# Kernel optimization log

Measured on AMD Instinct MI355X. Metric: run time of the kernel, lower is better.

## Reference

```python
import jax, jax.numpy as jnp
import numpy as np

N = 10000      # num_nodes
E = 640000     # num_edges
D = 256        # in_channels
POOL_SIZES = [(N, 48), (48, 12), (12, 4), (4, 1)]


def gcn_conv(x, src, dst, ew, W, b, n):
    """PyG-style GCNConv with edge weights: add self-loops, symmetric norm, scatter-add."""
    loop = jnp.arange(n)
    s = jnp.concatenate([src, loop])
    d = jnp.concatenate([dst, loop])
    w = jnp.concatenate([ew, jnp.ones((n,), x.dtype)])
    deg = jax.ops.segment_sum(w, d, num_segments=n)
    dinv = jnp.where(deg > 0, deg ** -0.5, 0.0)
    norm = dinv[s] * w * dinv[d]                      # [E+N]
    h = x @ W                                         # [n, out]
    out = jax.ops.segment_sum(norm[:, None] * h[s], d, num_segments=n)
    return out + b


def diffpool(x, P):
    """Learned-assignment DiffPool: S=softmax(P); x'=S^T x; reg = mean row entropy of S."""
    S = jax.nn.softmax(P, axis=-1)                    # [n_in, n_out]
    xp = S.T @ x                                      # [n_out, feat]
    reg = jnp.mean(-jnp.sum(S * jnp.log(S + 1e-12), axis=-1))
    return xp, reg


def setup_inputs() -> dict:
    key = jax.random.key(0)
    ks = jax.random.split(key, 12)
    inp = {
        "x": jax.random.normal(ks[0], (N, D), jnp.float32),
        "edge_index": jax.random.randint(ks[1], (2, E), 0, N, jnp.int64),
        "edge_attr": jax.random.uniform(ks[2], (E, 1), jnp.float32),
        "adj": jax.random.uniform(ks[3], (N, N), jnp.float32),
        # GCNConv params (out channels hard-coded to 1 in the module)
        "W1": jax.random.normal(ks[4], (D, 1), jnp.float32) / np.sqrt(D),
        "b1": jnp.zeros((1,), jnp.float32),
        "W2": jax.random.normal(ks[5], (1, 1), jnp.float32),
        "b2": jnp.zeros((1,), jnp.float32),
    }
    for i, (ni, no) in enumerate(POOL_SIZES):
        inp[f"P{i+1}"] = jax.random.normal(ks[6 + i], (ni, no), jnp.float32) * 0.1
    return inp


def reference(x, edge_index, edge_attr, adj, W1, b1, W2, b2, P1, P2, P3, P4):
    src, dst = edge_index[0], edge_index[1]
    ew = edge_attr[:, 0]
    h1 = gcn_conv(x, src, dst, ew, W1, b1, N)                       # [N,1]
    h = jnp.concatenate([h1, gcn_conv(h1[:, -1:], src, dst, ew, W2, b2, N)], axis=-1)
    h = jnp.concatenate([h, gcn_conv(h[:, -1:], src, dst, ew, W2, b2, N)], axis=-1)  # [N,3]
    reg = jnp.float32(0.0)
    for P in (P1, P2, P3, P4):
        h, r = diffpool(h, P)
        reg = reg + r
    return (h, reg)                                                  # h: [1,3]
```

## Files before the change

### kernel.cpp

```cpp
#include <hip/hip_runtime.h>
#include <math.h>

#define NN 10000
#define EE 640000
#define DD 256
#define NBK 128
#define NPB 79
#define NWRT 256
#define EPW (EE / NWRT)
#define SLOT 48
#define CELLS (NBK * SLOT)
#define SPAN (NWRT * SLOT)
#define NDEG 64
#define EPD (EE / NDEG)
#define NTHR 512

#define OFF_DINV 0
#define OFF_XW   (NN)
#define OFF_C1   (2*NN)
#define OFF_C2   (3*NN)
#define OFF_XP   (4*NN)
#define OFF_S1   (4*NN + 160)
#define OFF_DEGP (OFF_S1 + 2*NBK*SPAN)
#define OFF_PA   (OFF_DEGP + NDEG*NN)
#define OFF_PB   (OFF_PA + NBK*NN)

__global__ __launch_bounds__(NTHR) void k1_sort_deg_xw(
    const int* __restrict__ src, const int* __restrict__ dst,
    const float* __restrict__ ew, const float* __restrict__ x,
    const float* __restrict__ W1, float* __restrict__ ws)
{
    __shared__ unsigned smem[12416];
    int tid = threadIdx.x, bid = blockIdx.x;
    int lane = tid & 63, wv = tid >> 6;
    if (bid < NWRT) {
        uint2* cells = (uint2*)smem;
        int*   curs  = (int*)(smem + 2 * CELLS);
        if (bid == 0 && tid < 160) ws[OFF_XP + tid] = 0.f;
        for (int i = tid; i < CELLS; i += NTHR) cells[i] = make_uint2(0u, 0u);
        if (tid < NBK) curs[tid] = 0;
        __syncthreads();
        int base = bid * EPW;
        for (int k = tid; k < EPW; k += NTHR) {
            int s = src[base + k], d = dst[base + k];
            float w = ew[base + k];
            int j = s / NPB, loc = s - j * NPB;
            int r = atomicAdd(&curs[j], 1);
            if (r < SLOT)
                cells[j * SLOT + r] =
                    make_uint2((unsigned)d | ((unsigned)loc << 14), __float_as_uint(w));
        }
        __syncthreads();
        uint2* S1 = (uint2*)(ws + OFF_S1);
        for (int i = tid; i < CELLS; i += NTHR) {
            int j = i / SLOT, r = i - j * SLOT;
            S1[((size_t)j * NWRT + bid) * SLOT + r] = cells[i];
        }
        if (bid < 250) {
            float4 wreg = reinterpret_cast<const float4*>(W1)[lane];
            #pragma unroll
            for (int rr = 0; rr < 5; ++rr) {
                int row = bid * 40 + wv * 5 + rr;
                float4 a = reinterpret_cast<const float4*>(x + (size_t)row * DD)[lane];
                float v = a.x*wreg.x + a.y*wreg.y + a.z*wreg.z + a.w*wreg.w;
                #pragma unroll
                for (int off = 32; off; off >>= 1) v += __shfl_xor(v, off);
                if (lane == 0) ws[OFF_XW + row] = v;
            }
        }
    } else {
        float* acc = (float*)smem;
        for (int i = tid; i < NN; i += NTHR) acc[i] = 0.f;
        __syncthreads();
        int base = (bid - NWRT) * EPD;
        for (int k = tid; k < EPD; k += NTHR)
            atomicAdd(&acc[dst[base + k]], ew[base + k]);
        __syncthreads();
        float* dp = ws + OFF_DEGP + (size_t)(bid - NWRT) * NN;
        for (int i = tid; i < NN; i += NTHR) dp[i] = acc[i];
    }
}

#define REDUCE_SLICES(PIN, NS)                                            \
    for (int n = lane; n < NPB; n += 64) {                                \
        float s = 0.f;                                                    \
        if (nbase + n < NN) {                                             \
            _Pragma("unroll")                                             \
            for (int q = 0; q < (NS); ++q)                                \
                s += (PIN)[(size_t)(wv * (NS) + q) * NN + nbase + n];     \
        }                                                                 \
        red[wv][n] = s;                                                   \
    }                                                                     \
    __syncthreads();

#define SCATTER_SPAN(POUT)                                                \
    {                                                                     \
        const uint2* span = (const uint2*)(ws + OFF_S1) + (size_t)bid * SPAN; \
        for (int k = tid; k < SPAN; k += NTHR) {                          \
            uint2 pk = span[k];                                           \
            float w = __uint_as_float(pk.y);                              \
            if (w != 0.f)                                                 \
                atomicAdd(&acc[pk.x & 0x3FFF], w * du[pk.x >> 14]);       \
        }                                                                 \
        __syncthreads();                                                  \
        float* pp = (POUT) + (size_t)bid * NN;                            \
        for (int i = tid; i < NN; i += NTHR) pp[i] = acc[i];              \
    }

__global__ __launch_bounds__(NTHR) void k2_dinv_scat1(float* __restrict__ ws)
{
    __shared__ float acc[NN];
    __shared__ float red[8][NPB];
    __shared__ float du[NPB];
    int tid = threadIdx.x, bid = blockIdx.x;
    int lane = tid & 63, wv = tid >> 6;
    int nbase = bid * NPB;
    int ncnt = min(NPB, NN - nbase);
    const float* pin = ws + OFF_DEGP;
    REDUCE_SLICES(pin, 8)
    if (tid < ncnt) {
        float tot = 1.f;
        #pragma unroll
        for (int q = 0; q < 8; ++q) tot += red[q][tid];
        float di = (tot > 0.f) ? 1.0f / sqrtf(tot) : 0.f;
        ws[OFF_DINV + nbase + tid] = di;
        du[tid] = di * ws[OFF_XW + nbase + tid];
    }
    for (int i = tid; i < NN; i += NTHR) acc[i] = 0.f;
    __syncthreads();
    SCATTER_SPAN(ws + OFF_PB)
}

__global__ __launch_bounds__(NTHR) void k_conv(
    const float* __restrict__ hin, const float* __restrict__ multp,
    const float* __restrict__ biasp, float* __restrict__ cout,
    const float* __restrict__ pin, float* __restrict__ pout,
    float* __restrict__ ws)
{
    __shared__ float acc[NN];
    __shared__ float red[8][NPB];
    __shared__ float du[NPB];
    int tid = threadIdx.x, bid = blockIdx.x;
    int lane = tid & 63, wv = tid >> 6;
    int nbase = bid * NPB;
    int ncnt = min(NPB, NN - nbase);
    REDUCE_SLICES(pin, 16)
    if (tid < ncnt) {
        float tot = 0.f;
        #pragma unroll
        for (int q = 0; q < 8; ++q) tot += red[q][tid];
        float di = ws[OFF_DINV + nbase + tid];
        float M = multp ? *multp : 1.0f;
        float cv = M * di * (tot + di * hin[nbase + tid]) + *biasp;
        cout[nbase + tid] = cv;
        du[tid] = di * cv;
    }
    for (int i = tid; i < NN; i += NTHR) acc[i] = 0.f;
    __syncthreads();
    SCATTER_SPAN(pout)
}

__global__ __launch_bounds__(NTHR) void k5_final(
    const float* __restrict__ multp, const float* __restrict__ biasp,
    const float* __restrict__ pin,
    const float* __restrict__ P1, const float* __restrict__ P2,
    const float* __restrict__ P3, float* __restrict__ ws, float* __restrict__ out)
{
    __shared__ float red[8][NPB];
    __shared__ float sc3[NPB];
    __shared__ float part[8][48][3];
    __shared__ float entW[8];
    __shared__ int sh_last;
    int tid = threadIdx.x, bid = blockIdx.x;
    int lane = tid & 63, wv = tid >> 6;
    int nbase = bid * NPB;
    int ncnt = min(NPB, NN - nbase);
    const float* c1 = ws + OFF_C1;
    const float* c2 = ws + OFF_C2;
    REDUCE_SLICES(pin, 16)
    if (tid < ncnt) {
        float tot = 0.f;
        #pragma unroll
        for (int q = 0; q < 8; ++q) tot += red[q][tid];
        float di = ws[OFF_DINV + nbase + tid];
        sc3[tid] = (*multp) * di * (tot + di * c2[nbase + tid]) + *biasp;
    }
    __syncthreads();
    float a0 = 0.f, a1 = 0.f, a2 = 0.f, ent = 0.f;
    for (int r = 0; r < 10; ++r) {
        int l = wv * 10 + r;
        if (l < ncnt) {
            int row = nbase + l;
            float pv = (lane < 48) ? P1[(size_t)row * 48 + lane] : -1e30f;
            float mx = pv;
            #pragma unroll
            for (int off = 32; off; off >>= 1) mx = fmaxf(mx, __shfl_xor(mx, off));
            float e = (lane < 48) ? expf(pv - mx) : 0.f;
            float sum = e;
            #pragma unroll
            for (int off = 32; off; off >>= 1) sum += __shfl_xor(sum, off);
            float p = e / sum;
            if (lane < 48) {
                ent -= p * logf(p + 1e-12f);
                a0 += p * c1[row];
                a1 += p * c2[row];
                a2 += p * sc3[l];
            }
        }
    }
    #pragma unroll
    for (int off = 32; off; off >>= 1) ent += __shfl_xor(ent, off);
    if (lane == 0) entW[wv] = ent;
    if (lane < 48) { part[wv][lane][0] = a0; part[wv][lane][1] = a1; part[wv][lane][2] = a2; }
    __syncthreads();
    float* xp1 = ws + OFF_XP;
    if (tid < 144) {
        int j = tid / 3, col = tid % 3;
        float sp = 0.f;
        #pragma unroll
        for (int w = 0; w < 8; ++w) sp += part[w][j][col];
        atomicAdd(&xp1[j * 3 + col], sp);
    }
    if (tid == 0) {
        float sp = 0.f;
        #pragma unroll
        for (int w = 0; w < 8; ++w) sp += entW[w];
        atomicAdd(&xp1[144], sp);
    }
    if (tid == 0) {
        __threadfence();
        int old = atomicAdd((int*)ws + OFF_XP + 152, 1);
        sh_last = (old == (int)gridDim.x - 1) ? 1 : 0;
    }
    __syncthreads();
    if (sh_last) {
        __shared__ float shXp[145];
        __shared__ float S2[48][12], xp2[12][3];
        __shared__ float S3[12][4], xp3[4][3];
        __shared__ float ent2, ent3;
        if (tid < 145) shXp[tid] = atomicAdd(&xp1[tid], 0.0f);
        if (tid == 0) { ent2 = 0.f; ent3 = 0.f; }
        __syncthreads();
        if (tid < 48) {
            float v[12], mx = -1e30f;
            #pragma unroll
            for (int j = 0; j < 12; j++) { v[j] = P2[tid * 12 + j]; mx = fmaxf(mx, v[j]); }
            float sm = 0.f;
            #pragma unroll
            for (int j = 0; j < 12; j++) { v[j] = expf(v[j] - mx); sm += v[j]; }
            float e = 0.f;
            #pragma unroll
            for (int j = 0; j < 12; j++) {
                float p = v[j] / sm; S2[tid][j] = p; e -= p * logf(p + 1e-12f);
            }
            atomicAdd(&ent2, e);
        }
        __syncthreads();
        if (tid < 36) {
            int j = tid / 3, col = tid % 3;
            float sm = 0.f;
            for (int i = 0; i < 48; i++) sm += S2[i][j] * shXp[i * 3 + col];
            xp2[j][col] = sm;
        }
        __syncthreads();
        if (tid < 12) {
            float v[4], mx = -1e30f;
            #pragma unroll
            for (int j = 0; j < 4; j++) { v[j] = P3[tid * 4 + j]; mx = fmaxf(mx, v[j]); }
            float sm = 0.f;
            #pragma unroll
            for (int j = 0; j < 4; j++) { v[j] = expf(v[j] - mx); sm += v[j]; }
            float e = 0.f;
            #pragma unroll
            for (int j = 0; j < 4; j++) {
                float p = v[j] / sm; S3[tid][j] = p; e -= p * logf(p + 1e-12f);
            }
            atomicAdd(&ent3, e);
        }
        __syncthreads();
        if (tid < 12) {
            int j = tid / 3, col = tid % 3;
            float sm = 0.f;
            for (int i = 0; i < 12; i++) sm += S3[i][j] * xp2[i][col];
            xp3[j][col] = sm;
        }
        __syncthreads();
        if (tid == 0) {
            float o0 = 0.f, o1 = 0.f, o2 = 0.f;
            for (int i = 0; i < 4; i++) {
                o0 += xp3[i][0]; o1 += xp3[i][1]; o2 += xp3[i][2];
            }
            float reg = shXp[144] / (float)NN + ent2 / 48.f + ent3 / 12.f;
            out[0] = o0; out[1] = o1; out[2] = o2; out[3] = reg;
        }
    }
}

extern "C" void kernel_launch(void* const* d_in, const int* in_sizes, int n_in,
                              void* d_out, int out_size, void* d_ws, size_t ws_size,
                              hipStream_t stream) {
    const float* x  = (const float*)d_in[0];
    const int*   ei = (const int*)d_in[1];
    const float* ea = (const float*)d_in[2];
    const float* W1 = (const float*)d_in[4];
    const float* b1 = (const float*)d_in[5];
    const float* W2 = (const float*)d_in[6];
    const float* b2 = (const float*)d_in[7];
    const float* P1 = (const float*)d_in[8];
    const float* P2 = (const float*)d_in[9];
    const float* P3 = (const float*)d_in[10];
    const int* src = ei;
    const int* dst = ei + EE;
    float* ws  = (float*)d_ws;
    float* out = (float*)d_out;

    float* xw    = ws + OFF_XW;
    float* c1    = ws + OFF_C1;
    float* c2    = ws + OFF_C2;
    float* partA = ws + OFF_PA;
    float* partB = ws + OFF_PB;

    k1_sort_deg_xw<<<NWRT + NDEG, NTHR, 0, stream>>>(src, dst, ea, x, W1, ws);
    k2_dinv_scat1<<<NBK, NTHR, 0, stream>>>(ws);
    k_conv<<<NBK, NTHR, 0, stream>>>(xw, nullptr, b1, c1, partB, partA, ws);
    k_conv<<<NBK, NTHR, 0, stream>>>(c1, W2, b2, c2, partA, partB, ws);
    k5_final<<<NBK, NTHR, 0, stream>>>(W2, b2, partB, P1, P2, P3, ws, out);
}
```

Measured before the change: 93.35 us.

## Replace padded per-writer edge slots with compacted counting-sorted bucket lists

The source-bucketing pass now does an in-block counting sort and appends each bucket's edges contiguously into a global per-bucket list, using a global atomic cursor that is zeroed by a memset before launch. The scatter kernels then read only the real edges rather than a padded span of fixed 48-entry slots per writer block, and no longer need a zero-weight check. Bucket count rises from 128 to 250 (40 nodes each), so the later stages launch more blocks but must reduce across twice as many partial slices. Bucket capacity is fixed at 3072 with no overflow check, which relies on the random edge distribution.

```diff
diff --git a/kernel.cpp b/kernel.cpp
--- a/kernel.cpp
+++ b/kernel.cpp
@@ -4,13 +4,11 @@
 #define NN 10000
 #define EE 640000
 #define DD 256
-#define NBK 128
-#define NPB 79
+#define NBK 250
+#define NPB 40
 #define NWRT 256
 #define EPW (EE / NWRT)
-#define SLOT 48
-#define CELLS (NBK * SLOT)
-#define SPAN (NWRT * SLOT)
+#define MAXB 3072
 #define NDEG 64
 #define EPD (EE / NDEG)
 #define NTHR 512
@@ -20,8 +18,9 @@
 #define OFF_C1   (2*NN)
 #define OFF_C2   (3*NN)
 #define OFF_XP   (4*NN)
-#define OFF_S1   (4*NN + 160)
-#define OFF_DEGP (OFF_S1 + 2*NBK*SPAN)
+#define OFF_GCUR (4*NN + 160)
+#define OFF_S1   (4*NN + 416)
+#define OFF_DEGP (OFF_S1 + 2*NBK*MAXB)
 #define OFF_PA   (OFF_DEGP + NDEG*NN)
 #define OFF_PB   (OFF_PA + NBK*NN)
 
@@ -30,37 +29,74 @@
     const float* __restrict__ ew, const float* __restrict__ x,
     const float* __restrict__ W1, float* __restrict__ ws)
 {
-    __shared__ unsigned smem[12416];
+    __shared__ unsigned raw[11392];
     int tid = threadIdx.x, bid = blockIdx.x;
     int lane = tid & 63, wv = tid >> 6;
     if (bid < NWRT) {
-        uint2* cells = (uint2*)smem;
-        int*   curs  = (int*)(smem + 2 * CELLS);
+        unsigned* s_key  = raw;
+        float*    s_val  = (float*)(raw + EPW);
+        unsigned* s_okey = raw + 2 * EPW;
+        float*    s_oval = (float*)(raw + 3 * EPW);
+        int* s_cnt   = (int*)(raw + 10000);
+        int* s_sincl = (int*)(raw + 10256);
+        int* s_baseL = (int*)(raw + 10512);
+        int* s_lcur  = (int*)(raw + 10768);
+        int* s_posg  = (int*)(raw + 11024);
+        int* s_wtot  = (int*)(raw + 11280);
         if (bid == 0 && tid < 160) ws[OFF_XP + tid] = 0.f;
-        for (int i = tid; i < CELLS; i += NTHR) cells[i] = make_uint2(0u, 0u);
-        if (tid < NBK) curs[tid] = 0;
+        if (tid < 256) s_cnt[tid] = 0;
         __syncthreads();
         int base = bid * EPW;
         for (int k = tid; k < EPW; k += NTHR) {
             int s = src[base + k], d = dst[base + k];
-            float w = ew[base + k];
             int j = s / NPB, loc = s - j * NPB;
-            int r = atomicAdd(&curs[j], 1);
-            if (r < SLOT)
-                cells[j * SLOT + r] =
-                    make_uint2((unsigned)d | ((unsigned)loc << 14), __float_as_uint(w));
+            s_key[k] = (unsigned)d | ((unsigned)loc << 14) | ((unsigned)j << 20);
+            s_val[k] = ew[base + k];
+            atomicAdd(&s_cnt[j], 1);
+        }
+        __syncthreads();
+        if (tid < 256) {
+            int v = s_cnt[tid];
+            int incl = v;
+            #pragma unroll
+            for (int off = 1; off < 64; off <<= 1) {
+                int t = __shfl_up(incl, off);
+                if (lane >= off) incl += t;
+            }
+            s_sincl[tid] = incl;
+            if (lane == 63) s_wtot[tid >> 6] = incl;
+        }
+        __syncthreads();
+        int* gcur = (int*)(ws + OFF_GCUR);
+        if (tid < 256) {
+            int w = tid >> 6, pre = 0;
+            for (int q = 0; q < w; ++q) pre += s_wtot[q];
+            int b = pre + s_sincl[tid] - s_cnt[tid];
+            s_baseL[tid] = b;
+            s_lcur[tid] = b;
+            if (tid < NBK) s_posg[tid] = atomicAdd(&gcur[tid], s_cnt[tid]);
+        }
+        __syncthreads();
+        for (int k = tid; k < EPW; k += NTHR) {
+            unsigned ky = s_key[k];
+            int j = ky >> 20;
+            int r = atomicAdd(&s_lcur[j], 1);
+            s_okey[r] = ky & 0xFFFFFu;
+            s_oval[r] = s_val[k];
         }
         __syncthreads();
         uint2* S1 = (uint2*)(ws + OFF_S1);
-        for (int i = tid; i < CELLS; i += NTHR) {
-            int j = i / SLOT, r = i - j * SLOT;
-            S1[((size_t)j * NWRT + bid) * SLOT + r] = cells[i];
-        }
-        if (bid < 250) {
+        for (int j = wv; j < NBK; j += 8) {
+            int c = s_cnt[j], bl = s_baseL[j];
+            size_t gb = (size_t)j * MAXB + s_posg[j];
+            for (int k = lane; k < c; k += 64)
+                S1[gb + k] = make_uint2(s_okey[bl + k], __float_as_uint(s_oval[bl + k]));
+        }
+        if (bid < NBK) {
             float4 wreg = reinterpret_cast<const float4*>(W1)[lane];
             #pragma unroll
             for (int rr = 0; rr < 5; ++rr) {
-                int row = bid * 40 + wv * 5 + rr;
+                int row = bid * NPB + wv * 5 + rr;
                 float4 a = reinterpret_cast<const float4*>(x + (size_t)row * DD)[lane];
                 float v = a.x*wreg.x + a.y*wreg.y + a.z*wreg.z + a.w*wreg.w;
                 #pragma unroll
@@ -69,7 +105,7 @@
             }
         }
     } else {
-        float* acc = (float*)smem;
+        float* acc = (float*)raw;
         for (int i = tid; i < NN; i += NTHR) acc[i] = 0.f;
         __syncthreads();
         int base = (bid - NWRT) * EPD;
@@ -81,30 +117,18 @@
     }
 }
 
-#define REDUCE_SLICES(PIN, NS)                                            \
-    for (int n = lane; n < NPB; n += 64) {                                \
-        float s = 0.f;                                                    \
-        if (nbase + n < NN) {                                             \
-            _Pragma("unroll")                                             \
-            for (int q = 0; q < (NS); ++q)                                \
-                s += (PIN)[(size_t)(wv * (NS) + q) * NN + nbase + n];     \
-        }                                                                 \
-        red[wv][n] = s;                                                   \
-    }                                                                     \
-    __syncthreads();
-
-#define SCATTER_SPAN(POUT)                                                \
-    {                                                                     \
-        const uint2* span = (const uint2*)(ws + OFF_S1) + (size_t)bid * SPAN; \
-        for (int k = tid; k < SPAN; k += NTHR) {                          \
-            uint2 pk = span[k];                                           \
-            float w = __uint_as_float(pk.y);                              \
-            if (w != 0.f)                                                 \
-                atomicAdd(&acc[pk.x & 0x3FFF], w * du[pk.x >> 14]);       \
-        }                                                                 \
-        __syncthreads();                                                  \
-        float* pp = (POUT) + (size_t)bid * NN;                            \
-        for (int i = tid; i < NN; i += NTHR) pp[i] = acc[i];              \
+#define SCATTER_SPAN(POUT)                                                   \
+    {                                                                        \
+        const uint2* span = (const uint2*)(ws + OFF_S1) + (size_t)bid * MAXB;\
+        int glen = ((const int*)(ws + OFF_GCUR))[bid];                       \
+        for (int k = tid; k < glen; k += NTHR) {                             \
+            uint2 pk = span[k];                                              \
+            atomicAdd(&acc[pk.x & 0x3FFF],                                   \
+                      __uint_as_float(pk.y) * du[pk.x >> 14]);               \
+        }                                                                    \
+        __syncthreads();                                                     \
+        float* pp = (POUT) + (size_t)bid * NN;                               \
+        for (int i = tid; i < NN; i += NTHR) pp[i] = acc[i];                 \
     }
 
 __global__ __launch_bounds__(NTHR) void k2_dinv_scat1(float* __restrict__ ws)
@@ -115,10 +139,16 @@
     int tid = threadIdx.x, bid = blockIdx.x;
     int lane = tid & 63, wv = tid >> 6;
     int nbase = bid * NPB;
-    int ncnt = min(NPB, NN - nbase);
-    const float* pin = ws + OFF_DEGP;
-    REDUCE_SLICES(pin, 8)
-    if (tid < ncnt) {
+    const float* dp = ws + OFF_DEGP;
+    if (lane < NPB) {
+        float s = 0.f;
+        #pragma unroll
+        for (int q = 0; q < 8; ++q)
+            s += dp[(size_t)(wv * 8 + q) * NN + nbase + lane];
+        red[wv][lane] = s;
+    }
+    __syncthreads();
+    if (tid < NPB) {
         float tot = 1.f;
         #pragma unroll
         for (int q = 0; q < 8; ++q) tot += red[q][tid];
@@ -128,7 +158,7 @@
     }
     for (int i = tid; i < NN; i += NTHR) acc[i] = 0.f;
     __syncthreads();
-    SCATTER_SPAN(ws + OFF_PB)
+    SCATTER_SPAN(ws + OFF_PA)
 }
 
 __global__ __launch_bounds__(NTHR) void k_conv(
@@ -143,9 +173,16 @@
     int tid = threadIdx.x, bid = blockIdx.x;
     int lane = tid & 63, wv = tid >> 6;
     int nbase = bid * NPB;
-    int ncnt = min(NPB, NN - nbase);
-    REDUCE_SLICES(pin, 16)
-    if (tid < ncnt) {
+    if (lane < NPB) {
+        float s = 0.f;
+        for (int qq = 0; qq < 32; ++qq) {
+            int sl = wv * 32 + qq;
+            if (sl < NBK) s += pin[(size_t)sl * NN + nbase + lane];
+        }
+        red[wv][lane] = s;
+    }
+    __syncthreads();
+    if (tid < NPB) {
         float tot = 0.f;
         #pragma unroll
         for (int q = 0; q < 8; ++q) tot += red[q][tid];
@@ -174,11 +211,18 @@
     int tid = threadIdx.x, bid = blockIdx.x;
     int lane = tid & 63, wv = tid >> 6;
     int nbase = bid * NPB;
-    int ncnt = min(NPB, NN - nbase);
     const float* c1 = ws + OFF_C1;
     const float* c2 = ws + OFF_C2;
-    REDUCE_SLICES(pin, 16)
-    if (tid < ncnt) {
+    if (lane < NPB) {
+        float s = 0.f;
+        for (int qq = 0; qq < 32; ++qq) {
+            int sl = wv * 32 + qq;
+            if (sl < NBK) s += pin[(size_t)sl * NN + nbase + lane];
+        }
+        red[wv][lane] = s;
+    }
+    __syncthreads();
+    if (tid < NPB) {
         float tot = 0.f;
         #pragma unroll
         for (int q = 0; q < 8; ++q) tot += red[q][tid];
@@ -187,25 +231,24 @@
     }
     __syncthreads();
     float a0 = 0.f, a1 = 0.f, a2 = 0.f, ent = 0.f;
-    for (int r = 0; r < 10; ++r) {
-        int l = wv * 10 + r;
-        if (l < ncnt) {
-            int row = nbase + l;
-            float pv = (lane < 48) ? P1[(size_t)row * 48 + lane] : -1e30f;
-            float mx = pv;
-            #pragma unroll
-            for (int off = 32; off; off >>= 1) mx = fmaxf(mx, __shfl_xor(mx, off));
-            float e = (lane < 48) ? expf(pv - mx) : 0.f;
-            float sum = e;
-            #pragma unroll
-            for (int off = 32; off; off >>= 1) sum += __shfl_xor(sum, off);
-            float p = e / sum;
-            if (lane < 48) {
-                ent -= p * logf(p + 1e-12f);
-                a0 += p * c1[row];
-                a1 += p * c2[row];
-                a2 += p * sc3[l];
-            }
+    #pragma unroll
+    for (int r = 0; r < 5; ++r) {
+        int l = wv * 5 + r;
+        int row = nbase + l;
+        float pv = (lane < 48) ? P1[(size_t)row * 48 + lane] : -1e30f;
+        float mx = pv;
+        #pragma unroll
+        for (int off = 32; off; off >>= 1) mx = fmaxf(mx, __shfl_xor(mx, off));
+        float e = (lane < 48) ? expf(pv - mx) : 0.f;
+        float sum = e;
+        #pragma unroll
+        for (int off = 32; off; off >>= 1) sum += __shfl_xor(sum, off);
+        float p = e / sum;
+        if (lane < 48) {
+            ent -= p * logf(p + 1e-12f);
+            a0 += p * c1[row];
+            a1 += p * c2[row];
+            a2 += p * sc3[l];
         }
     }
     #pragma unroll
@@ -320,9 +363,10 @@
     float* partA = ws + OFF_PA;
     float* partB = ws + OFF_PB;
 
+    hipMemsetAsync(ws + OFF_GCUR, 0, 256 * sizeof(int), stream);
     k1_sort_deg_xw<<<NWRT + NDEG, NTHR, 0, stream>>>(src, dst, ea, x, W1, ws);
     k2_dinv_scat1<<<NBK, NTHR, 0, stream>>>(ws);
-    k_conv<<<NBK, NTHR, 0, stream>>>(xw, nullptr, b1, c1, partB, partA, ws);
-    k_conv<<<NBK, NTHR, 0, stream>>>(c1, W2, b2, c2, partA, partB, ws);
-    k5_final<<<NBK, NTHR, 0, stream>>>(W2, b2, partB, P1, P2, P3, ws, out);
-}
+    k_conv<<<NBK, NTHR, 0, stream>>>(xw, nullptr, b1, c1, partA, partB, ws);
+    k_conv<<<NBK, NTHR, 0, stream>>>(c1, W2, b2, c2, partB, partA, ws);
+    k5_final<<<NBK, NTHR, 0, stream>>>(W2, b2, partA, P1, P2, P3, ws, out);
+}
```

Measured after the change: 110.0 us. 17.9% more time.
